# Performance work log

Measured on AMD Instinct MI355X. Metric: run time of the kernel, lower is better.

The kernel has to match this reference:

```python
import jax, jax.numpy as jnp
import numpy as np

# Constructor constants (init_kwargs)
DT = 0.01
M = 1.0
C = 0.1


def setup_inputs() -> dict:
    key = jax.random.key(0)
    k1, = jax.random.split(key, 1)
    B, T = 4096, 4096
    inputs = jax.random.uniform(k1, (B, T, 2), dtype=jnp.float32)  # [...,0]=k (stiffness), [...,1]=F
    xdot_init = jnp.zeros((B, 1), dtype=jnp.float32)
    x_init = jnp.zeros((B, 1), dtype=jnp.float32)
    return {"inputs": inputs, "xdot_init": xdot_init, "x_init": x_init}


def _rk4_step(carry, inp):
    # carry: (xdot0, x0) each [B,1]; inp: [B,2]
    xdot0, x0 = carry
    k = inp[:, 0:1]
    F = inp[:, 1:2]
    dt = DT
    halfdt = 0.5 * dt

    def f(xdot, x):
        xddot = (-C * xdot - k * x + F) / M
        return xddot, xdot

    xdot1, x1 = f(xdot0, x0)
    xdot2, x2 = f(xdot0 + halfdt * xdot1, x0 + halfdt * x1)
    xdot3, x3 = f(xdot0 + halfdt * xdot2, x0 + halfdt * x2)
    xdot4, x4 = f(xdot0 + dt * xdot3, x0 + dt * x3)
    xdot = xdot0 + dt / 6 * (xdot1 + 2 * xdot2 + 2 * xdot3 + xdot4)
    x = x0 + dt / 6 * (x1 + 2 * x2 + 2 * x3 + x4)
    xddot = (-C * xdot - k * x + F) / M  # cell output
    return (xdot, x), xddot


def reference(inputs, xdot_init, x_init):
    # inputs: [B, T, 2] -> scan over time with carry states [B,1]
    seq = jnp.transpose(inputs, (1, 0, 2))  # [T, B, 2]
    (_, _), xddot_seq = jax.lax.scan(_rk4_step, (xdot_init, x_init), seq)
    # xddot_seq: [T, B, 1] -> [B, T, 1] (RNN return_sequences output)
    return jnp.transpose(xddot_seq, (1, 0, 2))
```

## Files before the change

### kernel.cpp

```cpp
#include <hip/hip_runtime.h>


#define TPB 256
#define STEPS 16
#define NWAVE (TPB / 64)

constexpr double dh = 0.01;
constexpr double dA = -0.1;

constexpr float DTF = (float)dh;
constexpr float AF  = (float)dA;

constexpr float cQ0 = (float)(dh + dA*dh*dh/2.0 + dA*dA*dh*dh*dh/6.0 + dA*dA*dA*dh*dh*dh*dh/24.0);
constexpr float cQ1 = (float)(-(dh*dh*dh/6.0 + dA*dh*dh*dh*dh/12.0));
constexpr float cP1 = (float)(-(dh*dh/2.0 + dA*dh*dh*dh/6.0 + dA*dA*dh*dh*dh*dh/24.0));
constexpr float cP2 = (float)(dh*dh*dh*dh/24.0);
constexpr float cS0 = (float)(dh*dh/2.0 + dA*dh*dh*dh/6.0 + dA*dA*dh*dh*dh*dh/24.0);
constexpr float cS1 = (float)(-dh*dh*dh*dh/24.0);
constexpr float cT1 = (float)(-(dh*dh*dh/6.0 + dA*dh*dh*dh*dh/24.0));

struct Xf { float a11, a12, a21, a22, bv, bx; };

struct StepRR { float R11, R12, R21, R22, rv, rx; };

__device__ __forceinline__ StepRR makeStep(float k, float F) {
    StepRR s;
    float Q  = fmaf(cQ1, k, cQ0);
    float P  = fmaf(fmaf(cP2, k, cP1), k, 1.0f);
    s.R11 = fmaf(AF, Q, P);
    s.R12 = -k * Q;
    s.R21 = Q;
    s.R22 = P;
    float Qs = fmaf(cS1, k, cS0);
    float Ps = fmaf(cT1, k, DTF);
    s.rv = F * fmaf(AF, Qs, Ps);
    s.rx = F * Qs;
    return s;
}

__device__ __forceinline__ Xf combine(const Xf& e, const Xf& l) {
    Xf r;
    r.a11 = fmaf(l.a11, e.a11, l.a12 * e.a21);
    r.a12 = fmaf(l.a11, e.a12, l.a12 * e.a22);
    r.a21 = fmaf(l.a21, e.a11, l.a22 * e.a21);
    r.a22 = fmaf(l.a21, e.a12, l.a22 * e.a22);
    r.bv  = fmaf(l.a11, e.bv, fmaf(l.a12, e.bx, l.bv));
    r.bx  = fmaf(l.a21, e.bv, fmaf(l.a22, e.bx, l.bx));
    return r;
}

__device__ __forceinline__ void foldStep(Xf& t, float k, float F) {
    StepRR s = makeStep(k, F);
    float a11 = fmaf(s.R11, t.a11, s.R12 * t.a21);
    float a12 = fmaf(s.R11, t.a12, s.R12 * t.a22);
    float a21 = fmaf(s.R21, t.a11, s.R22 * t.a21);
    float a22 = fmaf(s.R21, t.a12, s.R22 * t.a22);
    float bv  = fmaf(s.R11, t.bv, fmaf(s.R12, t.bx, s.rv));
    float bx  = fmaf(s.R21, t.bv, fmaf(s.R22, t.bx, s.rx));
    t.a11 = a11; t.a12 = a12; t.a21 = a21; t.a22 = a22; t.bv = bv; t.bx = bx;
}

__device__ __forceinline__ float stepState(float& v, float& x, float k, float F) {
    StepRR s = makeStep(k, F);
    float vn = fmaf(s.R11, v, fmaf(s.R12, x, s.rv));
    float xn = fmaf(s.R21, v, fmaf(s.R22, x, s.rx));
    v = vn; x = xn;
    return fmaf(AF, vn, fmaf(-k, xn, F));
}

__device__ __forceinline__ Xf shflUp(const Xf& t, int d) {
    Xf r;
    r.a11 = __shfl_up(t.a11, d);
    r.a12 = __shfl_up(t.a12, d);
    r.a21 = __shfl_up(t.a21, d);
    r.a22 = __shfl_up(t.a22, d);
    r.bv  = __shfl_up(t.bv, d);
    r.bx  = __shfl_up(t.bx, d);
    return r;
}

__global__ __launch_bounds__(TPB) void spring_scan_kernel(
    const float* __restrict__ in, const float* __restrict__ v0g,
    const float* __restrict__ x0g, float* __restrict__ out, int T) {
    const int b    = blockIdx.x;
    const int j    = threadIdx.x;
    const int lane = j & 63;
    const int wave = j >> 6;

    const float4* in4 = (const float4*)(in + (size_t)b * (size_t)T * 2);
    float4 kf[STEPS / 2];
#pragma unroll
    for (int i = 0; i < STEPS / 2; ++i) kf[i] = in4[(size_t)j * (STEPS / 2) + i];

    Xf t = {1.f, 0.f, 0.f, 1.f, 0.f, 0.f};
#pragma unroll
    for (int i = 0; i < STEPS / 2; ++i) {
        foldStep(t, kf[i].x, kf[i].y);
        foldStep(t, kf[i].z, kf[i].w);
    }

#pragma unroll
    for (int d = 1; d < 64; d <<= 1) {
        Xf o = shflUp(t, d);
        if (lane >= d) t = combine(o, t);
    }

    __shared__ Xf wtot[NWAVE];
    if (lane == 63) wtot[wave] = t;
    Xf ex = shflUp(t, 1);
    __syncthreads();
    Xf pre = {1.f, 0.f, 0.f, 1.f, 0.f, 0.f};
#pragma unroll
    for (int w = 0; w < NWAVE - 1; ++w) {
        if (w < wave) pre = combine(pre, wtot[w]);
    }
    Xf myex = (lane == 0) ? pre : combine(pre, ex);

    float v0 = v0g[b], x0 = x0g[b];
    float v = fmaf(myex.a11, v0, fmaf(myex.a12, x0, myex.bv));
    float x = fmaf(myex.a21, v0, fmaf(myex.a22, x0, myex.bx));

    float4 ov[STEPS / 4];
    float* op = (float*)ov;
#pragma unroll
    for (int i = 0; i < STEPS / 2; ++i) {
        op[2 * i]     = stepState(v, x, kf[i].x, kf[i].y);
        op[2 * i + 1] = stepState(v, x, kf[i].z, kf[i].w);
    }
    float4* out4 = (float4*)(out + (size_t)b * (size_t)T);
#pragma unroll
    for (int i = 0; i < STEPS / 4; ++i) out4[(size_t)j * (STEPS / 4) + i] = ov[i];
}

__global__ void spring_naive_kernel(const float* __restrict__ in,
                                    const float* __restrict__ v0g,
                                    const float* __restrict__ x0g,
                                    float* __restrict__ out, int B, int T) {
    int b = blockIdx.x * blockDim.x + threadIdx.x;
    if (b >= B) return;
    const float dt = 0.01f, half = 0.005f, C = 0.1f;
    float v = v0g[b], x = x0g[b];
    const float* p = in + (size_t)b * (size_t)T * 2;
    float* o = out + (size_t)b * (size_t)T;
    for (int tt = 0; tt < T; ++tt) {
        float k = p[2 * tt], F = p[2 * tt + 1];
        float a1 = F - C * v - k * x;                   float s1 = v;
        float v2 = v + half * a1, x2 = x + half * s1;
        float a2 = F - C * v2 - k * x2;                 float s2 = v2;
        float v3 = v + half * a2, x3 = x + half * s2;
        float a3 = F - C * v3 - k * x3;                 float s3 = v3;
        float v4 = v + dt * a3,  x4 = x + dt * s3;
        float a4 = F - C * v4 - k * x4;                 float s4 = v4;
        v = v + dt / 6.f * (a1 + 2.f * a2 + 2.f * a3 + a4);
        x = x + dt / 6.f * (s1 + 2.f * s2 + 2.f * s3 + s4);
        o[tt] = F - C * v - k * x;
    }
}

extern "C" void kernel_launch(void* const* d_in, const int* in_sizes, int n_in,
                              void* d_out, int out_size, void* d_ws, size_t ws_size,
                              hipStream_t stream) {
    const float* in  = (const float*)d_in[0];
    const float* v0g = (const float*)d_in[1];
    const float* x0g = (const float*)d_in[2];
    float* out = (float*)d_out;

    const int B = in_sizes[1];
    const int T = in_sizes[0] / (2 * B);

    if (T == TPB * STEPS) {
        spring_scan_kernel<<<B, TPB, 0, stream>>>(in, v0g, x0g, out, T);
    } else {
        int tpb = 256;
        spring_naive_kernel<<<(B + tpb - 1) / tpb, tpb, 0, stream>>>(in, v0g, x0g, out, B, T);
    }
}
```

Baseline: 215.0 us.

## Stage input and output through padded LDS for fully coalesced global access

```diff
diff --git a/kernel.cpp b/kernel.cpp
--- a/kernel.cpp
+++ b/kernel.cpp
@@ -20,7 +20,6 @@
 constexpr float cT1 = (float)(-(dh*dh*dh/6.0 + dA*dh*dh*dh*dh/24.0));
 
 struct Xf { float a11, a12, a21, a22, bv, bx; };
-
 struct StepRR { float R11, R12, R21, R22, rv, rx; };
 
 __device__ __forceinline__ StepRR makeStep(float k, float F) {
@@ -83,20 +82,30 @@
     const float* __restrict__ in, const float* __restrict__ v0g,
     const float* __restrict__ x0g, float* __restrict__ out, int T) {
     const int b    = blockIdx.x;
-    const int j    = threadIdx.x;
-    const int lane = j & 63;
-    const int wave = j >> 6;
+    const int tid  = threadIdx.x;
+    const int lane = tid & 63;
+    const int wave = tid >> 6;
+
+    __shared__ float lds[8704];
+    __shared__ Xf wtot[NWAVE];
 
     const float4* in4 = (const float4*)(in + (size_t)b * (size_t)T * 2);
-    float4 kf[STEPS / 2];
 #pragma unroll
-    for (int i = 0; i < STEPS / 2; ++i) kf[i] = in4[(size_t)j * (STEPS / 2) + i];
+    for (int it = 0; it < 8; ++it) {
+        int e4 = tid + TPB * it;
+        float4 vv = in4[e4];
+        int L = 4 * e4 + 2 * (e4 >> 3);
+        *(float2*)&lds[L]     = make_float2(vv.x, vv.y);
+        *(float2*)&lds[L + 2] = make_float2(vv.z, vv.w);
+    }
+    __syncthreads();
 
+    const int base = 34 * tid;
     Xf t = {1.f, 0.f, 0.f, 1.f, 0.f, 0.f};
 #pragma unroll
-    for (int i = 0; i < STEPS / 2; ++i) {
-        foldStep(t, kf[i].x, kf[i].y);
-        foldStep(t, kf[i].z, kf[i].w);
+    for (int m = 0; m < STEPS; ++m) {
+        float2 kf = *(const float2*)&lds[base + 2 * m];
+        foldStep(t, kf.x, kf.y);
     }
 
 #pragma unroll
@@ -105,7 +114,6 @@
         if (lane >= d) t = combine(o, t);
     }
 
-    __shared__ Xf wtot[NWAVE];
     if (lane == 63) wtot[wave] = t;
     Xf ex = shflUp(t, 1);
     __syncthreads();
@@ -120,16 +128,26 @@
     float v = fmaf(myex.a11, v0, fmaf(myex.a12, x0, myex.bv));
     float x = fmaf(myex.a21, v0, fmaf(myex.a22, x0, myex.bx));
 
-    float4 ov[STEPS / 4];
-    float* op = (float*)ov;
 #pragma unroll
-    for (int i = 0; i < STEPS / 2; ++i) {
-        op[2 * i]     = stepState(v, x, kf[i].x, kf[i].y);
-        op[2 * i + 1] = stepState(v, x, kf[i].z, kf[i].w);
+    for (int m = 0; m < STEPS; ++m) {
+        float2 kf = *(const float2*)&lds[base + 2 * m];
+        float xdd = stepState(v, x, kf.x, kf.y);
+        lds[base + 2 * m] = xdd;
     }
+    __syncthreads();
+
     float4* out4 = (float4*)(out + (size_t)b * (size_t)T);
 #pragma unroll
-    for (int i = 0; i < STEPS / 4; ++i) out4[(size_t)j * (STEPS / 4) + i] = ov[i];
+    for (int i = 0; i < 4; ++i) {
+        int e0 = 4 * tid + 1024 * i;
+        int Lb = 34 * (e0 >> 4) + 2 * (e0 & 15);
+        float4 o;
+        o.x = lds[Lb];
+        o.y = lds[Lb + 2];
+        o.z = lds[Lb + 4];
+        o.w = lds[Lb + 6];
+        out4[tid + TPB * i] = o;
+    }
 }
 
 __global__ void spring_naive_kernel(const float* __restrict__ in,
```

New measurement: 212.2 us, median of 2. No clear change (-1.3%).
